# Kernel tuning notes

Measured on AMD Instinct MI355X. Metric: run time of the kernel, lower is better.

## Reference

```python
import jax, jax.numpy as jnp
import numpy as np

B, S, H, V, E, C = 32, 512, 512, 32000, 768, 3
D = E + C  # LSTM input dim = embedding + one-hot prior


def setup_inputs() -> dict:
    key = jax.random.key(0)
    ks = jax.random.split(key, 13)
    p = lambda k, shape: (jax.random.normal(k, shape, jnp.float32) * 0.02)
    return {
        "embedding_table": p(ks[0], (V, E)),
        "fwd_kernel": p(ks[1], (D, 4 * H)),
        "fwd_rec_kernel": p(ks[2], (H, 4 * H)),
        "fwd_bias": p(ks[3], (4 * H,)),
        "bwd_kernel": p(ks[4], (D, 4 * H)),
        "bwd_rec_kernel": p(ks[5], (H, 4 * H)),
        "bwd_bias": p(ks[6], (4 * H,)),
        "w1": p(ks[7], (2 * H, H)),
        "b1": jnp.zeros((H,), jnp.float32),
        "w2": p(ks[8], (H, C)),
        "b2": jnp.zeros((C,), jnp.float32),
        "input_ids": jax.random.randint(ks[9], (B, S), 0, V),
        "prior_info": jax.random.randint(ks[10], (B, S), 0, C),
        "labels": jax.random.randint(ks[11], (B, S), 0, C),
    }


def _lstm(x, K, R, b, reverse):
    """Keras-style LSTM (gate order i,f,c,o). x: [B,S,D] -> [B,S,H].
    With reverse=True, lax.scan processes time backwards and emits outputs
    aligned to original positions, matching Keras Bidirectional's
    go_backwards + output re-reversal."""
    zx = jnp.einsum('bsd,dh->bsh', x, K) + b  # input projection, [B,S,4H]
    zx = jnp.swapaxes(zx, 0, 1)               # [S,B,4H]
    h0 = jnp.zeros((x.shape[0], R.shape[0]), x.dtype)

    def step(carry, z):
        h, c = carry
        z = z + h @ R
        i, f, g, o = jnp.split(z, 4, axis=-1)
        c = jax.nn.sigmoid(f) * c + jax.nn.sigmoid(i) * jnp.tanh(g)
        h = jax.nn.sigmoid(o) * jnp.tanh(c)
        return (h, c), h

    _, ys = jax.lax.scan(step, (h0, h0), zx, reverse=reverse)
    return jnp.swapaxes(ys, 0, 1)  # [B,S,H]


def reference(embedding_table, fwd_kernel, fwd_rec_kernel, fwd_bias,
              bwd_kernel, bwd_rec_kernel, bwd_bias,
              w1, b1, w2, b2, input_ids, prior_info, labels):
    emb = embedding_table[input_ids]                       # [B,S,E] gather
    prior = jax.nn.one_hot(prior_info, C, dtype=emb.dtype)  # [B,S,3]
    x = jnp.concatenate([emb, prior], axis=-1)             # [B,S,771]
    hf = _lstm(x, fwd_kernel, fwd_rec_kernel, fwd_bias, reverse=False)
    hb = _lstm(x, bwd_kernel, bwd_rec_kernel, bwd_bias, reverse=True)
    h = jnp.concatenate([hf, hb], axis=-1)                 # [B,S,2H]
    h = h @ w1 + b1                                        # Dense (linear)
    logits = h @ w2 + b2                                   # [B,S,3]
    probs = jax.nn.softmax(logits, axis=-1)
    logp = jax.nn.log_softmax(logits, axis=-1)
    lab = jax.nn.one_hot(labels, C, dtype=logp.dtype)
    loss = jnp.mean(-jnp.sum(logp * lab, axis=(-1, -2)))
    return probs, loss
```

## Files before the change

### kernel.cpp

```cpp
#include <hip/hip_runtime.h>
#include <hip/hip_bf16.h>

#define BB 32
#define SS 512
#define HH 512
#define VV 32000
#define EE 768
#define NC 3
#define G4 2048
#define MM (BB*SS)
#define SENT 0xFFFFFFFFu

typedef __attribute__((ext_vector_type(8))) short bf16x8;
typedef __attribute__((ext_vector_type(4))) float f32x4;
typedef unsigned int u32;
typedef unsigned short u16;
typedef unsigned long long u64;
typedef __attribute__((ext_vector_type(4))) u32 u32x4;

#define MFMA(a,b,c) __builtin_amdgcn_mfma_f32_16x16x32_bf16(a,b,c,0,0,0)

static __device__ __forceinline__ u16 f2bf(float f) {
  union { float f; u32 u; } v; v.f = f;
  return (u16)((v.u + 0x7fffu + ((v.u >> 16) & 1u)) >> 16);
}
static __device__ __forceinline__ float bf2f(u16 h) {
  union { u32 u; float f; } v; v.u = ((u32)h) << 16;
  return v.f;
}
static __device__ __forceinline__ float sigm(float x) { return 1.f/(1.f+__expf(-x)); }
static __device__ __forceinline__ float tanh_f(float x) {
  x = fminf(8.f, fmaxf(-8.f, x));
  float t = __expf(2.f*x);
  return (t-1.f)/(t+1.f);
}

__global__ void k_conv(const float* __restrict__ src, u16* __restrict__ dst, int n8) {
  int i = blockIdx.x * blockDim.x + threadIdx.x;
  if (i >= n8) return;
  const float4* s = ((const float4*)src) + (size_t)i*2;
  float4 a = s[0], b = s[1];
  u32 x = (u32)f2bf(a.x) | ((u32)f2bf(a.y) << 16);
  u32 y = (u32)f2bf(a.z) | ((u32)f2bf(a.w) << 16);
  u32 z = (u32)f2bf(b.x) | ((u32)f2bf(b.y) << 16);
  u32 w = (u32)f2bf(b.z) | ((u32)f2bf(b.w) << 16);
  ((uint4*)dst)[i] = make_uint4(x, y, z, w);
}

__global__ void k_pack(const float* __restrict__ src, u16* __restrict__ dst, int K, int N) {
  int tid = blockIdx.x * 256 + threadIdx.x;
  int nkf = K >> 5;
  int l = tid & 63, fi = tid >> 6;
  int kf = fi % nkf, nf = fi / nkf;
  if (nf >= (N >> 4)) return;
  int col = nf * 16 + (l & 15);
  int k0 = kf * 32 + (l >> 4) * 8;
  u32 o[4];
  #pragma unroll
  for (int j = 0; j < 4; ++j) {
    u16 lo = f2bf(src[(size_t)(k0 + 2*j) * N + col]);
    u16 hi = f2bf(src[(size_t)(k0 + 2*j + 1) * N + col]);
    o[j] = (u32)lo | ((u32)hi << 16);
  }
  *((uint4*)(dst + (size_t)tid * 8)) = make_uint4(o[0], o[1], o[2], o[3]);
}

__global__ __launch_bounds__(256) void k_proj(
    const u16* __restrict__ embT, const u16* __restrict__ Bp0, const u16* __restrict__ Bp1,
    const float* __restrict__ bias0, const float* __restrict__ bias1,
    const float* __restrict__ K0, const float* __restrict__ K1,
    const int* __restrict__ ids, const int* __restrict__ prior,
    u16* __restrict__ zx0, u16* __restrict__ zx1)
{
  int mt = blockIdx.x;
  int gy = blockIdx.y;
  int dir = gy >> 4, nt = gy & 15;
  const u16* Bp = dir ? Bp1 : Bp0;
  const float* bias = dir ? bias1 : bias0;
  const float* Kp = (dir ? K1 : K0) + (size_t)EE * G4;
  u16* zx = dir ? zx1 : zx0;
  int w = threadIdx.x >> 6, l = threadIdx.x & 63;
  int m0 = mt * 128 + w * 32;
  int r0 = m0 + (l & 15);
  int id0 = ids[(r0 & 31) * SS + (r0 >> 5)];
  int id1 = ids[((r0 + 16) & 31) * SS + ((r0 + 16) >> 5)];
  const u16* a0p = embT + (size_t)id0 * EE + (l >> 4) * 8;
  const u16* a1p = embT + (size_t)id1 * EE + (l >> 4) * 8;
  f32x4 acc[2][8];
  #pragma unroll
  for (int i = 0; i < 2; ++i)
    #pragma unroll
    for (int j = 0; j < 8; ++j) acc[i][j] = (f32x4){0.f,0.f,0.f,0.f};
  const u16* bbase = Bp + ((size_t)(nt*8)*24)*512 + (size_t)l*8;
  for (int kf = 0; kf < 24; ++kf) {
    bf16x8 a0 = *(const bf16x8*)(a0p + kf*32);
    bf16x8 a1 = *(const bf16x8*)(a1p + kf*32);
    #pragma unroll
    for (int nf = 0; nf < 8; ++nf) {
      bf16x8 bv = *(const bf16x8*)(bbase + (size_t)(nf*24 + kf)*512);
      acc[0][nf] = MFMA(a0, bv, acc[0][nf]);
      acc[1][nf] = MFMA(a1, bv, acc[1][nf]);
    }
  }
  int cb = nt*128 + (l & 15);
  #pragma unroll
  for (int mi = 0; mi < 2; ++mi) {
    #pragma unroll
    for (int r = 0; r < 4; ++r) {
      int row = m0 + mi*16 + (l >> 4)*4 + r;
      int p = prior[(row & 31) * SS + (row >> 5)];
      const float* kr = Kp + (size_t)p * G4;
      u16* zr = zx + (size_t)row * G4;
      #pragma unroll
      for (int nf = 0; nf < 8; ++nf) {
        int col = cb + nf*16;
        zr[col] = f2bf(acc[mi][nf][r] + bias[col] + kr[col]);
      }
    }
  }
}

__global__ __launch_bounds__(512, 2) void k_scan(
    const u16* __restrict__ zxf, const u16* __restrict__ zxb,
    const u16* __restrict__ Rf, const u16* __restrict__ Rb,
    u16* __restrict__ hf, u16* __restrict__ hb)
{
  int wg = blockIdx.x, dir = wg >> 4, wgi = wg & 15;
  const u16* zx = dir ? zxb : zxf;
  const u16* Rp = dir ? Rb : Rf;
  u16* hbuf = dir ? hb : hf;
  int tid = threadIdx.x;
  int w = tid >> 6, l = tid & 63;
  int g = w & 3, ch = w >> 2;
  int ncb = g*32 + wgi*2 + ch;
  bf16x8 rb[16];
  #pragma unroll
  for (int kf = 0; kf < 16; ++kf)
    rb[kf] = *(const bf16x8*)(Rp + (((size_t)ncb*16 + kf)*64 + l)*8);

  __shared__ char hstage[32*1040];
  __shared__ float zbuf[4][32][33];

  int eb = tid >> 4;
  int ec = (tid & 15) * 2;
  const char* sread0 = hstage + (l & 15)*1040 + (l >> 4)*16;
  const char* sread1 = sread0 + 16*1040;
  char* swrite = hstage + (tid >> 4)*1040 + (tid & 15)*16;
  size_t goff = (size_t)(tid >> 4)*1024 + (tid & 15)*16;

  float c0 = 0.f, c1 = 0.f;
  for (int step = 0; step < SS; ++step) {
    int t = dir ? (SS - 1 - step) : step;
    const u32* zxr = (const u32*)(zx + ((size_t)t*BB + eb)*G4 + wgi*32 + ec);
    u32 xi = zxr[0];
    u32 xf = zxr[256];
    u32 xg = zxr[512];
    u32 xo = zxr[768];
    f32x4 acc0 = {0.f,0.f,0.f,0.f}, acc1 = {0.f,0.f,0.f,0.f};
    if (step > 0) {
      int tp = dir ? t + 1 : t - 1;
      const char* gsrc = (const char*)(hbuf + (size_t)tp*BB*HH) + goff;
      u32x4 s0v, s1v, s2v, s3v;
      for (;;) {
        asm volatile("global_load_dwordx4 %0, %1, off sc0 sc1" : "=v"(s0v) : "v"(gsrc)     : "memory");
        asm volatile("global_load_dwordx4 %0, %1, off sc0 sc1" : "=v"(s1v) : "v"(gsrc+256) : "memory");
        asm volatile("global_load_dwordx4 %0, %1, off sc0 sc1" : "=v"(s2v) : "v"(gsrc+512) : "memory");
        asm volatile("global_load_dwordx4 %0, %1, off sc0 sc1" : "=v"(s3v) : "v"(gsrc+768) : "memory");
        asm volatile("s_waitcnt vmcnt(0)" ::: "memory");
        bool ok = s0v[0]!=SENT && s0v[1]!=SENT && s0v[2]!=SENT && s0v[3]!=SENT
               && s1v[0]!=SENT && s1v[1]!=SENT && s1v[2]!=SENT && s1v[3]!=SENT
               && s2v[0]!=SENT && s2v[1]!=SENT && s2v[2]!=SENT && s2v[3]!=SENT
               && s3v[0]!=SENT && s3v[1]!=SENT && s3v[2]!=SENT && s3v[3]!=SENT;
        if (ok) break;
        __builtin_amdgcn_s_sleep(1);
      }
      __builtin_amdgcn_sched_barrier(0);
      *(u32x4*)(swrite)       = s0v;
      *(u32x4*)(swrite + 256) = s1v;
      *(u32x4*)(swrite + 512) = s2v;
      *(u32x4*)(swrite + 768) = s3v;
      __syncthreads();
      #pragma unroll
      for (int kf = 0; kf < 16; ++kf) {
        bf16x8 a0 = *(const bf16x8*)(sread0 + kf*64);
        bf16x8 a1 = *(const bf16x8*)(sread1 + kf*64);
        acc0 = MFMA(a0, rb[kf], acc0);
        acc1 = MFMA(a1, rb[kf], acc1);
      }
    }
    int zc = ch*16 + (l & 15);
    int zb0 = (l >> 4) * 4;
    #pragma unroll
    for (int r = 0; r < 4; ++r) {
      zbuf[g][zc][zb0 + r] = acc0[r];
      zbuf[g][zc][16 + zb0 + r] = acc1[r];
    }
    __syncthreads();
    float zi0 = zbuf[0][ec  ][eb] + bf2f((u16)(xi & 0xffffu));
    float zi1 = zbuf[0][ec+1][eb] + bf2f((u16)(xi >> 16));
    float zf0 = zbuf[1][ec  ][eb] + bf2f((u16)(xf & 0xffffu));
    float zf1 = zbuf[1][ec+1][eb] + bf2f((u16)(xf >> 16));
    float zg0 = zbuf[2][ec  ][eb] + bf2f((u16)(xg & 0xffffu));
    float zg1 = zbuf[2][ec+1][eb] + bf2f((u16)(xg >> 16));
    float zo0 = zbuf[3][ec  ][eb] + bf2f((u16)(xo & 0xffffu));
    float zo1 = zbuf[3][ec+1][eb] + bf2f((u16)(xo >> 16));
    c0 = sigm(zf0)*c0 + sigm(zi0)*tanh_f(zg0);
    c1 = sigm(zf1)*c1 + sigm(zi1)*tanh_f(zg1);
    float h0 = sigm(zo0)*tanh_f(c0);
    float h1 = sigm(zo1)*tanh_f(c1);
    u32 hpk = (u32)f2bf(h0) | ((u32)f2bf(h1) << 16);
    u32* hp = (u32*)(hbuf + ((size_t)t*BB + eb)*HH + wgi*32 + ec);
    asm volatile("global_store_dword %0, %1, off sc0 sc1" :: "v"(hp), "v"(hpk) : "memory");
  }
}

__global__ __launch_bounds__(256) void k_dense(
    const u16* __restrict__ hf, const u16* __restrict__ hb,
    const u16* __restrict__ w1p, const float* __restrict__ b1,
    u16* __restrict__ h1)
{
  int mt = blockIdx.x, nt = blockIdx.y;
  int w = threadIdx.x >> 6, l = threadIdx.x & 63;
  int m0 = mt*128 + w*32;
  int r0 = m0 + (l & 15);
  const u16* f0 = hf + (size_t)r0*HH + (l >> 4)*8;
  const u16* f1 = hf + (size_t)(r0+16)*HH + (l >> 4)*8;
  const u16* g0 = hb + (size_t)r0*HH + (l >> 4)*8;
  const u16* g1 = hb + (size_t)(r0+16)*HH + (l >> 4)*8;
  f32x4 acc[2][8];
  #pragma unroll
  for (int i = 0; i < 2; ++i)
    #pragma unroll
    for (int j = 0; j < 8; ++j) acc[i][j] = (f32x4){0.f,0.f,0.f,0.f};
  const u16* bbase = w1p + ((size_t)(nt*8)*32)*512 + (size_t)l*8;
  for (int kf = 0; kf < 32; ++kf) {
    const u16* s0 = (kf < 16) ? (f0 + kf*32) : (g0 + (kf-16)*32);
    const u16* s1 = (kf < 16) ? (f1 + kf*32) : (g1 + (kf-16)*32);
    bf16x8 a0 = *(const bf16x8*)s0;
    bf16x8 a1 = *(const bf16x8*)s1;
    #pragma unroll
    for (int nf = 0; nf < 8; ++nf) {
      bf16x8 bv = *(const bf16x8*)(bbase + (size_t)(nf*32 + kf)*512);
      acc[0][nf] = MFMA(a0, bv, acc[0][nf]);
      acc[1][nf] = MFMA(a1, bv, acc[1][nf]);
    }
  }
  int cb = nt*128 + (l & 15);
  #pragma unroll
  for (int mi = 0; mi < 2; ++mi) {
    #pragma unroll
    for (int r = 0; r < 4; ++r) {
      int row = m0 + mi*16 + (l >> 4)*4 + r;
      #pragma unroll
      for (int nf = 0; nf < 8; ++nf) {
        int col = cb + nf*16;
        h1[(size_t)row*HH + col] = f2bf(acc[mi][nf][r] + b1[col]);
      }
    }
  }
}

__global__ __launch_bounds__(256) void k_out(
    const u16* __restrict__ h1, const float* __restrict__ w2, const float* __restrict__ b2,
    const int* __restrict__ labels, float* __restrict__ out, float* __restrict__ part)
{
  int w = threadIdx.x >> 6, l = threadIdx.x & 63;
  float w2r[8][3];
  #pragma unroll
  for (int i = 0; i < 8; ++i)
    #pragma unroll
    for (int c = 0; c < 3; ++c) w2r[i][c] = w2[(l*8 + i)*3 + c];
  float b20 = b2[0], b21 = b2[1], b22 = b2[2];
  float nll = 0.f;
  int base = (blockIdx.x*4 + w)*16;
  for (int r = 0; r < 16; ++r) {
    int row = base + r;
    bf16x8 hv = *(const bf16x8*)(h1 + (size_t)row*HH + l*8);
    float s0 = 0.f, s1 = 0.f, s2 = 0.f;
    #pragma unroll
    for (int i = 0; i < 8; ++i) {
      float x = bf2f((u16)hv[i]);
      s0 += x*w2r[i][0]; s1 += x*w2r[i][1]; s2 += x*w2r[i][2];
    }
    #pragma unroll
    for (int off = 32; off > 0; off >>= 1) {
      s0 += __shfl_down(s0, off);
      s1 += __shfl_down(s1, off);
      s2 += __shfl_down(s2, off);
    }
    if (l == 0) {
      float l0 = s0+b20, l1 = s1+b21, l2 = s2+b22;
      float m = fmaxf(l0, fmaxf(l1, l2));
      float e0 = __expf(l0-m), e1 = __expf(l1-m), e2 = __expf(l2-m);
      float Z = e0+e1+e2, inv = 1.f/Z;
      int b = row & 31, s = row >> 5;
      float* po = out + ((size_t)b*SS + s)*3;
      po[0] = e0*inv; po[1] = e1*inv; po[2] = e2*inv;
      int lab = labels[b*SS + s];
      float ll = (lab == 0) ? l0 : (lab == 1 ? l1 : l2);
      nll += (m + __logf(Z)) - ll;
    }
  }
  __shared__ float ps[4];
  if (l == 0) ps[w] = nll;
  __syncthreads();
  if (threadIdx.x == 0) part[blockIdx.x] = ps[0]+ps[1]+ps[2]+ps[3];
}

__global__ void k_loss(const float* __restrict__ part, float* __restrict__ out) {
  __shared__ float sh[256];
  sh[threadIdx.x] = part[threadIdx.x];
  __syncthreads();
  for (int s = 128; s > 0; s >>= 1) {
    if (threadIdx.x < s) sh[threadIdx.x] += sh[threadIdx.x + s];
    __syncthreads();
  }
  if (threadIdx.x == 0) out[(size_t)MM*NC] = sh[0] / (float)BB;
}

extern "C" void kernel_launch(void* const* d_in, const int* in_sizes, int n_in,
                              void* d_out, int out_size, void* d_ws, size_t ws_size,
                              hipStream_t stream) {
  (void)in_sizes; (void)n_in; (void)out_size;
  const float* emb = (const float*)d_in[0];
  const float* fK  = (const float*)d_in[1];
  const float* fR  = (const float*)d_in[2];
  const float* fb  = (const float*)d_in[3];
  const float* bK  = (const float*)d_in[4];
  const float* bR  = (const float*)d_in[5];
  const float* bb  = (const float*)d_in[6];
  const float* w1  = (const float*)d_in[7];
  const float* b1  = (const float*)d_in[8];
  const float* w2  = (const float*)d_in[9];
  const float* b2  = (const float*)d_in[10];
  const int* ids   = (const int*)d_in[11];
  const int* prior = (const int*)d_in[12];
  const int* labels= (const int*)d_in[13];

  size_t off = 0;
  auto take = [&](size_t bytes) -> char* {
    char* p = (char*)d_ws + off;
    off += (bytes + 255) & ~(size_t)255;
    return p;
  };
  u16* embT = (u16*)take((size_t)VV*EE*2);
  u16* Kfp  = (u16*)take((size_t)EE*G4*2);
  u16* Kbp  = (u16*)take((size_t)EE*G4*2);
  u16* Rfp  = (u16*)take((size_t)HH*G4*2);
  u16* Rbp  = (u16*)take((size_t)HH*G4*2);
  u16* w1p  = (u16*)take((size_t)(2*HH)*HH*2);
  u16* zxf  = (u16*)take((size_t)MM*G4*2);
  u16* zxb  = (u16*)take((size_t)MM*G4*2);
  u16* hf   = (u16*)take((size_t)MM*HH*2);
  u16* hb   = (u16*)take((size_t)MM*HH*2);
  u16* h1   = (u16*)take((size_t)MM*HH*2);
  float* part = (float*)take(256*4);
  if (off > ws_size) return;

  hipMemsetAsync(hf, 0xFF, (size_t)MM*HH*2, stream);
  hipMemsetAsync(hb, 0xFF, (size_t)MM*HH*2, stream);
  k_conv<<<12000, 256, 0, stream>>>(emb, embT, VV*EE/8);
  k_pack<<<768, 256, 0, stream>>>(fK, Kfp, EE, G4);
  k_pack<<<768, 256, 0, stream>>>(bK, Kbp, EE, G4);
  k_pack<<<512, 256, 0, stream>>>(fR, Rfp, HH, G4);
  k_pack<<<512, 256, 0, stream>>>(bR, Rbp, HH, G4);
  k_pack<<<256, 256, 0, stream>>>(w1, w1p, 2*HH, HH);
  k_proj<<<dim3(128,32), 256, 0, stream>>>(embT, Kfp, Kbp, fb, bb, fK, bK, ids, prior, zxf, zxb);
  k_scan<<<32, 512, 0, stream>>>(zxf, zxb, Rfp, Rbp, hf, hb);
  k_dense<<<dim3(128,4), 256, 0, stream>>>(hf, hb, w1p, b1, h1);
  k_out<<<256, 256, 0, stream>>>(h1, w2, b2, labels, (float*)d_out, part);
  k_loss<<<1, 256, 0, stream>>>(part, (float*)d_out);
}
```

Baseline: 2.207 ms.

## Load recurrent h MFMA fragments directly from global, drop LDS staging

Each wave now loads its own A-fragment of the previous hidden state straight from global memory into registers, 16 dwordx4 per lane, instead of cooperatively staging it through a shared-memory buffer. The work split changes so each wave covers a half of the batch rows across both column blocks, holding two sets of recurrent-weight fragments. This removes the LDS write, a barrier and the LDS reads from the serial per-step critical path. In exchange it issues four times more global traffic per step, doubles the register footprint of the resident weights, and makes the sentinel poll wave-wide.

```diff
diff --git a/kernel.cpp b/kernel.cpp
--- a/kernel.cpp
+++ b/kernel.cpp
@@ -131,22 +131,20 @@
   u16* hbuf = dir ? hb : hf;
   int tid = threadIdx.x;
   int w = tid >> 6, l = tid & 63;
-  int g = w & 3, ch = w >> 2;
-  int ncb = g*32 + wgi*2 + ch;
-  bf16x8 rb[16];
-  #pragma unroll
-  for (int kf = 0; kf < 16; ++kf)
-    rb[kf] = *(const bf16x8*)(Rp + (((size_t)ncb*16 + kf)*64 + l)*8);
-
-  __shared__ char hstage[32*1040];
+  int g = w & 3, bh = w >> 2;
+  int ncb0 = g*32 + wgi*2;
+  bf16x8 rb0[16], rb1[16];
+  #pragma unroll
+  for (int kf = 0; kf < 16; ++kf) {
+    rb0[kf] = *(const bf16x8*)(Rp + (((size_t)ncb0*16 + kf)*64 + l)*8);
+    rb1[kf] = *(const bf16x8*)(Rp + (((size_t)(ncb0+1)*16 + kf)*64 + l)*8);
+  }
+
   __shared__ float zbuf[4][32][33];
 
   int eb = tid >> 4;
   int ec = (tid & 15) * 2;
-  const char* sread0 = hstage + (l & 15)*1040 + (l >> 4)*16;
-  const char* sread1 = sread0 + 16*1040;
-  char* swrite = hstage + (tid >> 4)*1040 + (tid & 15)*16;
-  size_t goff = (size_t)(tid >> 4)*1024 + (tid & 15)*16;
+  const char* afbase = (const char*)(hbuf + (size_t)(bh*16 + (l & 15))*HH) + (l >> 4)*16;
 
   float c0 = 0.f, c1 = 0.f;
   for (int step = 0; step < SS; ++step) {
@@ -159,41 +157,38 @@
     f32x4 acc0 = {0.f,0.f,0.f,0.f}, acc1 = {0.f,0.f,0.f,0.f};
     if (step > 0) {
       int tp = dir ? t + 1 : t - 1;
-      const char* gsrc = (const char*)(hbuf + (size_t)tp*BB*HH) + goff;
-      u32x4 s0v, s1v, s2v, s3v;
+      const char* gsrc = afbase + (size_t)tp*BB*HH*2;
+      u32x4 av[16];
       for (;;) {
-        asm volatile("global_load_dwordx4 %0, %1, off sc0 sc1" : "=v"(s0v) : "v"(gsrc)     : "memory");
-        asm volatile("global_load_dwordx4 %0, %1, off sc0 sc1" : "=v"(s1v) : "v"(gsrc+256) : "memory");
-        asm volatile("global_load_dwordx4 %0, %1, off sc0 sc1" : "=v"(s2v) : "v"(gsrc+512) : "memory");
-        asm volatile("global_load_dwordx4 %0, %1, off sc0 sc1" : "=v"(s3v) : "v"(gsrc+768) : "memory");
+        #pragma unroll
+        for (int kf = 0; kf < 16; ++kf)
+          asm volatile("global_load_dwordx4 %0, %1, off sc0 sc1"
+                       : "=v"(av[kf]) : "v"(gsrc + kf*64) : "memory");
         asm volatile("s_waitcnt vmcnt(0)" ::: "memory");
-        bool ok = s0v[0]!=SENT && s0v[1]!=SENT && s0v[2]!=SENT && s0v[3]!=SENT
-               && s1v[0]!=SENT && s1v[1]!=SENT && s1v[2]!=SENT && s1v[3]!=SENT
-               && s2v[0]!=SENT && s2v[1]!=SENT && s2v[2]!=SENT && s2v[3]!=SENT
-               && s3v[0]!=SENT && s3v[1]!=SENT && s3v[2]!=SENT && s3v[3]!=SENT;
-        if (ok) break;
+        __builtin_amdgcn_sched_barrier(0);
+        bool ok = true;
+        #pragma unroll
+        for (int kf = 0; kf < 16; ++kf)
+          ok = ok && av[kf][0] != SENT && av[kf][1] != SENT
+                  && av[kf][2] != SENT && av[kf][3] != SENT;
+        if (!__any(!ok)) break;
         __builtin_amdgcn_s_sleep(1);
       }
       __builtin_amdgcn_sched_barrier(0);
-      *(u32x4*)(swrite)       = s0v;
-      *(u32x4*)(swrite + 256) = s1v;
-      *(u32x4*)(swrite + 512) = s2v;
-      *(u32x4*)(swrite + 768) = s3v;
-      __syncthreads();
       #pragma unroll
       for (int kf = 0; kf < 16; ++kf) {
-        bf16x8 a0 = *(const bf16x8*)(sread0 + kf*64);
-        bf16x8 a1 = *(const bf16x8*)(sread1 + kf*64);
-        acc0 = MFMA(a0, rb[kf], acc0);
-        acc1 = MFMA(a1, rb[kf], acc1);
+        union { u32x4 u; bf16x8 v; } cv; cv.u = av[kf];
+        acc0 = MFMA(cv.v, rb0[kf], acc0);
+        acc1 = MFMA(cv.v, rb1[kf], acc1);
       }
     }
-    int zc = ch*16 + (l & 15);
-    int zb0 = (l >> 4) * 4;
+    __syncthreads();
+    int zc = l & 15;
+    int zr = bh*16 + (l >> 4)*4;
     #pragma unroll
     for (int r = 0; r < 4; ++r) {
-      zbuf[g][zc][zb0 + r] = acc0[r];
-      zbuf[g][zc][16 + zb0 + r] = acc1[r];
+      zbuf[g][zc][zr + r]      = acc0[r];
+      zbuf[g][16 + zc][zr + r] = acc1[r];
     }
     __syncthreads();
     float zi0 = zbuf[0][ec  ][eb] + bf2f((u16)(xi & 0xffffu));
```

Result: slower. 3.968 ms (+79.8%).
